# Optimization experiments

Hardware: AMD Instinct MI355X
Metric: run time of the kernel (lower is better)

The kernel has to match this reference:

```python
import jax, jax.numpy as jnp
import numpy as np

N, E, H, L, T = 20000, 160000, 128, 4, 20


def _ln(x, g, b):
    m = jnp.mean(x, -1, keepdims=True)
    v = jnp.mean((x - m) ** 2, -1, keepdims=True)
    return (x - m) * jax.lax.rsqrt(v + 1e-5) * g + b


def _mlp(x, W1, b1, W2, b2, g, b):
    # Linear -> ReLU -> Linear -> LayerNorm, as in mlp_2layer
    h = jax.nn.relu(x @ W1 + b1)
    return _ln(h @ W2 + b2, g, b)


def setup_inputs() -> dict:
    key = jax.random.key(0)
    ks = iter(jax.random.split(key, 64))

    def W(shape):
        fan_in = shape[-2]
        return jax.random.normal(next(ks), shape, jnp.float32) * (fan_in ** -0.5)

    z = lambda s: jnp.zeros(s, jnp.float32)
    o = lambda s: jnp.ones(s, jnp.float32)

    inp = {
        'x': jax.random.normal(next(ks), (N, 12), jnp.float32),
        'edge_attr': jax.random.normal(next(ks), (E, 4), jnp.float32),
        'edge_index': jax.random.randint(next(ks), (2, E), 0, N),
        # node encoder (12 -> H)
        'Wn1': W((12, H)), 'bn1': z((H,)), 'Wn2': W((H, H)), 'bn2': z((H,)), 'gn_ln': o((H,)), 'bn_ln': z((H,)),
        # edge encoder (4 -> H)
        'We1': W((4, H)), 'be1': z((H,)), 'We2': W((H, H)), 'be2': z((H,)), 'ge_ln': o((H,)), 'be_ln': z((H,)),
        # stacked per-layer params: edge_mlp (4H -> H), node_mlp (3H -> H), global_mlp (3H -> H)
        'lEW1': W((L, 4 * H, H)), 'lEb1': z((L, H)), 'lEW2': W((L, H, H)), 'lEb2': z((L, H)), 'lEg': o((L, H)), 'lEbt': z((L, H)),
        'lVW1': W((L, 3 * H, H)), 'lVb1': z((L, H)), 'lVW2': W((L, H, H)), 'lVb2': z((L, H)), 'lVg': o((L, H)), 'lVbt': z((L, H)),
        'lGW1': W((L, 3 * H, H)), 'lGb1': z((L, H)), 'lGW2': W((L, H, H)), 'lGb2': z((L, H)), 'lGg': o((L, H)), 'lGbt': z((L, H)),
        # CNN output head: Conv1d(1->8,k=15,s=4) -> ReLU -> Conv1d(8->1,k=10,s=1)
        'c1w': jax.random.normal(next(ks), (8, 1, 15), jnp.float32) * 0.1, 'c1b': z((8,)),
        'c2w': jax.random.normal(next(ks), (1, 8, 10), jnp.float32) * 0.1, 'c2b': z((1,)),
    }
    return inp


def _forward(x, edge_attr, edge_index,
             Wn1, bn1, Wn2, bn2, gn_ln, bn_ln,
             We1, be1, We2, be2, ge_ln, be_ln,
             lEW1, lEb1, lEW2, lEb2, lEg, lEbt,
             lVW1, lVb1, lVW2, lVb2, lVg, lVbt,
             lGW1, lGb1, lGW2, lGb2, lGg, lGbt,
             c1w, c1b, c2w, c2b):
    senders = edge_index[0]
    receivers = edge_index[1]
    n_nodes = x.shape[0]
    n_edges = edge_attr.shape[0]

    x_v = _mlp(x, Wn1, bn1, Wn2, bn2, gn_ln, bn_ln)          # [N, H]
    x_e = _mlp(edge_attr, We1, be1, We2, be2, ge_ln, be_ln)  # [E, H]
    g = jnp.zeros((1, H), x_v.dtype)                          # B=1 global (no global inputs)

    def step(carry, p):
        x_v, x_e, g = carry
        (EW1, Eb1, EW2, Eb2, Eg, Ebt,
         VW1, Vb1, VW2, Vb2, Vg, Vbt,
         GW1, Gb1, GW2, Gb2, Gg, Gbt) = p
        # edge update: gather sender/receiver feats, concat with edge + global
        g_e = jnp.broadcast_to(g, (n_edges, H))
        edge_in = jnp.concatenate([x_v[senders], x_v[receivers], x_e, g_e], -1)  # [E, 4H]
        x_e = x_e + _mlp(edge_in, EW1, Eb1, EW2, Eb2, Eg, Ebt)
        # node update: sum-aggregate messages by receiver
        aggr = jax.ops.segment_sum(x_e, receivers, num_segments=n_nodes)  # [N, H]
        g_v = jnp.broadcast_to(g, (n_nodes, H))
        node_in = jnp.concatenate([x_v, aggr, g_v], -1)  # [N, 3H]
        x_v = x_v + _mlp(node_in, VW1, Vb1, VW2, Vb2, Vg, Vbt)
        # global update
        g_in = jnp.concatenate([jnp.sum(x_v, 0, keepdims=True), jnp.sum(x_e, 0, keepdims=True), g], -1)  # [1, 3H]
        g = g + _mlp(g_in, GW1, Gb1, GW2, Gb2, Gg, Gbt)
        return (x_v, x_e, g), None

    params = (lEW1, lEb1, lEW2, lEb2, lEg, lEbt,
              lVW1, lVb1, lVW2, lVb2, lVg, lVbt,
              lGW1, lGb1, lGW2, lGb2, lGg, lGbt)
    (x_v, x_e, g), _ = jax.lax.scan(step, (x_v, x_e, g), params)

    # CNN head over the H=128 feature axis -> [N, T]
    dn = ('NCH', 'OIH', 'NCH')
    h = x_v[:, None, :]  # [N, 1, 128]
    h = jax.lax.conv_general_dilated(h, c1w, (4,), 'VALID', dimension_numbers=dn)
    h = jax.nn.relu(h + c1b[None, :, None])  # [N, 8, 29]
    h = jax.lax.conv_general_dilated(h, c2w, (1,), 'VALID', dimension_numbers=dn) + c2b[None, :, None]
    return h[:, 0, :]  # [N, 20]


def reference(x, edge_attr, edge_index,
              Wn1, bn1, Wn2, bn2, gn_ln, bn_ln,
              We1, be1, We2, be2, ge_ln, be_ln,
              lEW1, lEb1, lEW2, lEb2, lEg, lEbt,
              lVW1, lVb1, lVW2, lVb2, lVg, lVbt,
              lGW1, lGb1, lGW2, lGb2, lGg, lGbt,
              c1w, c1b, c2w, c2b):
    return _forward(x, edge_attr, edge_index,
                    Wn1, bn1, Wn2, bn2, gn_ln, bn_ln,
                    We1, be1, We2, be2, ge_ln, be_ln,
                    lEW1, lEb1, lEW2, lEb2, lEg, lEbt,
                    lVW1, lVb1, lVW2, lVb2, lVg, lVbt,
                    lGW1, lGb1, lGW2, lGb2, lGg, lGbt,
                    c1w, c1b, c2w, c2b)
```

## Files before the change

### kernel.cpp

```cpp
#include <hip/hip_runtime.h>

#define NN 20000
#define NE 160000
#define HD 128
#define SA 136

typedef __attribute__((ext_vector_type(8))) short  bfrag;
typedef __attribute__((ext_vector_type(4))) short  s4v;
typedef __attribute__((ext_vector_type(4))) float  facc;
typedef __attribute__((ext_vector_type(4))) float  f4v;

__device__ __forceinline__ float bf2f(unsigned short u){
  union { unsigned int i; float f; } v; v.i = ((unsigned int)u) << 16; return v.f;
}
__device__ __forceinline__ unsigned short f2bf(float f){
  union { float f; unsigned int i; } v; v.f = f;
  unsigned int r = v.i + 0x7fffu + ((v.i >> 16) & 1u);
  return (unsigned short)(r >> 16);
}

__global__ void sentinel_kernel(float* out, float code){
  if (threadIdx.x < 32) out[threadIdx.x] = code;
}

__device__ __forceinline__ void gemm_tile(const short* Ab,
                                          const unsigned short* pk,
                                          int m0, int lane, facc acc[8]){
  const int q = lane >> 4, c = lane & 15;
  #pragma unroll
  for (int kt = 0; kt < 4; ++kt){
    bfrag a = *(const bfrag*)(Ab + (m0 + c) * SA + kt * 32 + q * 8);
    const bfrag* bp = (const bfrag*)pk + kt * 512 + lane;
    #pragma unroll
    for (int nt = 0; nt < 8; ++nt){
      acc[nt] = __builtin_amdgcn_mfma_f32_16x16x32_bf16(a, bp[nt * 64], acc[nt], 0, 0, 0);
    }
  }
}

__device__ __forceinline__ void gemm_tile_h(const short* Ab,
                                            const unsigned short* pk,
                                            int m0, int ntb, int lane, facc acc[4]){
  const int q = lane >> 4, c = lane & 15;
  #pragma unroll
  for (int kt = 0; kt < 4; ++kt){
    bfrag a = *(const bfrag*)(Ab + (m0 + c) * SA + kt * 32 + q * 8);
    const bfrag* bp = (const bfrag*)pk + kt * 512 + ntb * 64 + lane;
    #pragma unroll
    for (int nt = 0; nt < 4; ++nt){
      acc[nt] = __builtin_amdgcn_mfma_f32_16x16x32_bf16(a, bp[nt * 64], acc[nt], 0, 0, 0);
    }
  }
}

__global__ __launch_bounds__(256) void pack_all(
    const float* Wn2, const float* We2,
    const float* lEW1, const float* lEW2,
    const float* lVW1, const float* lVW2,
    unsigned short* packed)
{
  int job = blockIdx.x * 256 + threadIdx.x;
  int mat = job >> 12, r12 = job & 4095;
  int plane = r12 >> 11, r = r12 & 2047;
  int kt = r >> 9, nt = (r >> 6) & 7, lane = r & 63;
  const float* src;
  if (mat == 0) src = Wn2;
  else if (mat == 1) src = We2;
  else {
    int m2 = mat - 2, l = m2 / 7, t = m2 % 7;
    switch (t){
      case 0: src = lEW1 + ((size_t)l*512 +   0)*HD; break;
      case 1: src = lEW1 + ((size_t)l*512 + 128)*HD; break;
      case 2: src = lEW1 + ((size_t)l*512 + 256)*HD; break;
      case 3: src = lEW2 + (size_t)l*HD*HD;          break;
      case 4: src = lVW1 + ((size_t)l*384 +   0)*HD; break;
      case 5: src = lVW1 + ((size_t)l*384 + 128)*HD; break;
      default: src = lVW2 + (size_t)l*HD*HD;         break;
    }
  }
  int krow = kt*32 + (lane>>4)*8, col = nt*16 + (lane&15);
  unsigned short v[8];
  #pragma unroll
  for (int j = 0; j < 8; ++j){
    float w = src[(size_t)(krow + j)*HD + col];
    unsigned short h = f2bf(w);
    v[j] = plane ? f2bf(w - bf2f(h)) : h;
  }
  unsigned short* dst = packed + ((size_t)mat*2 + plane)*16384
                               + ((size_t)(kt*8+nt)*64 + lane)*8;
  #pragma unroll
  for (int j = 0; j < 8; ++j) dst[j] = v[j];
}

__global__ __launch_bounds__(128) void init_small(
    float* g, float* cbe, float* cbv, float* xvs, float* xes,
    const float* Eb1_0, const float* Vb1_0)
{
  int t = threadIdx.x;
  g[t] = 0.f; xvs[t] = 0.f; xes[t] = 0.f;
  cbe[t] = Eb1_0[t]; cbv[t] = Vb1_0[t];
}

__global__ __launch_bounds__(256) void zero_cnt(int* cnt){
  int i = blockIdx.x * 256 + threadIdx.x;
  if (i < NN) cnt[i] = 0;
}
__global__ __launch_bounds__(256) void hist_kernel(const int* eidx, int* cnt){
  int e = blockIdx.x * 256 + threadIdx.x;
  atomicAdd(&cnt[eidx[NE + e]], 1);
}
__global__ __launch_bounds__(1024) void scan_kernel(const int* cnt, int* base, int* ofs){
  __shared__ int wsum[16];
  int t = threadIdx.x, lane = t & 63;
  int vals[20]; int loc = 0;
  if (t < 1000){
    #pragma unroll
    for (int k = 0; k < 20; ++k){ vals[k] = cnt[t*20 + k]; loc += vals[k]; }
  }
  int inc = loc;
  #pragma unroll
  for (int d = 1; d < 64; d <<= 1){ int o = __shfl_up(inc, d); if (lane >= d) inc += o; }
  if (lane == 63) wsum[t >> 6] = inc;
  __syncthreads();
  if (t < 16){
    int v = wsum[t];
    #pragma unroll
    for (int d = 1; d < 16; d <<= 1){ int o = __shfl_up(v, d); if (t >= d) v += o; }
    wsum[t] = v;
  }
  __syncthreads();
  int woff = (t >= 64) ? wsum[(t >> 6) - 1] : 0;
  int run = woff + inc - loc;
  if (t < 1000){
    #pragma unroll
    for (int k = 0; k < 20; ++k){ base[t*20 + k] = run; ofs[t*20 + k] = run; run += vals[k]; }
  }
  if (t == 0) base[NN] = NE;
}
__global__ __launch_bounds__(256) void scatter_kernel(const int* eidx, int* ofs,
                                                      int* perm, int* ssid, int* srid){
  int e = blockIdx.x * 256 + threadIdx.x;
  int s = eidx[e], r = eidx[NE + e];
  int pos = atomicAdd(&ofs[r], 1);
  perm[pos] = e; ssid[pos] = s; srid[pos] = r;
}

__global__ __launch_bounds__(256) void enc_node(
    const float* x, const float* W1, const float* b1,
    const unsigned short* pkW2, const float* b2,
    const float* gl, const float* bl, float* xvf, int nrows)
{
  __shared__ float inb[64*12];
  __shared__ __align__(16) short Hh[64*SA];
  __shared__ __align__(16) short Hl[64*SA];
  int tid = threadIdx.x, r0 = blockIdx.x * 64;
  for (int j = tid; j < 64*12; j += 256){
    int rr = j / 12, k = j % 12, rg = r0 + rr;
    inb[j] = (rg < nrows) ? x[(size_t)rg*12 + k] : 0.f;
  }
  __syncthreads();
  {
    int cc = tid & 127;
    float w1c[12];
    #pragma unroll
    for (int k = 0; k < 12; ++k) w1c[k] = W1[k*HD + cc];
    float bb = b1[cc];
    for (int it = 0; it < 32; ++it){
      int rr = it*2 + (tid >> 7);
      float a = bb;
      #pragma unroll
      for (int k = 0; k < 12; ++k) a += inb[rr*12 + k] * w1c[k];
      float h = fmaxf(a, 0.f);
      unsigned short hh = f2bf(h);
      Hh[rr*SA + cc] = (short)hh;
      Hl[rr*SA + cc] = (short)f2bf(h - bf2f(hh));
    }
  }
  __syncthreads();
  int lane = tid & 63, q = lane >> 4, c = lane & 15, m0 = (tid >> 6) * 16;
  facc a2[8];
  #pragma unroll
  for (int nt = 0; nt < 8; ++nt) a2[nt] = (facc){0.f,0.f,0.f,0.f};
  gemm_tile(Hh, pkW2,         m0, lane, a2);
  gemm_tile(Hl, pkW2,         m0, lane, a2);
  gemm_tile(Hh, pkW2 + 16384, m0, lane, a2);
  #pragma unroll
  for (int i = 0; i < 4; ++i){
    int rl = m0 + q*4 + i, rg = r0 + rl;
    float vals[8], s = 0.f, ss = 0.f;
    #pragma unroll
    for (int nt = 0; nt < 8; ++nt){
      float v = a2[nt][i] + b2[nt*16 + c];
      vals[nt] = v; s += v; ss += v*v;
    }
    s += __shfl_xor(s,1); ss += __shfl_xor(ss,1);
    s += __shfl_xor(s,2); ss += __shfl_xor(ss,2);
    s += __shfl_xor(s,4); ss += __shfl_xor(ss,4);
    s += __shfl_xor(s,8); ss += __shfl_xor(ss,8);
    float mean = s * 0.0078125f;
    float var  = ss * 0.0078125f - mean*mean;
    float rs   = rsqrtf(var + 1e-5f);
    if (rg < nrows){
      #pragma unroll
      for (int nt = 0; nt < 8; ++nt){
        int col = nt*16 + c;
        xvf[(size_t)rg*HD + col] = (vals[nt]-mean)*rs*gl[col] + bl[col];
      }
    }
  }
}

__global__ __launch_bounds__(256) void enc_edge(
    const float* ea, const int* perm, const float* W1, const float* b1,
    const unsigned short* pkW2, const float* b2,
    const float* gl, const float* bl, unsigned short* xeb)
{
  __shared__ float inb[64*4];
  __shared__ __align__(16) short Hh[64*SA];
  __shared__ __align__(16) short Hl[64*SA];
  int tid = threadIdx.x, r0 = blockIdx.x * 64;
  {
    int rr = tid >> 2, k = tid & 3;
    int pe = perm[r0 + rr];
    inb[tid] = ea[(size_t)pe*4 + k];
  }
  __syncthreads();
  {
    int cc = tid & 127;
    float w0 = W1[0*HD+cc], w1 = W1[1*HD+cc], w2 = W1[2*HD+cc], w3 = W1[3*HD+cc];
    float bb = b1[cc];
    for (int it = 0; it < 32; ++it){
      int rr = it*2 + (tid >> 7);
      float a = bb + inb[rr*4+0]*w0 + inb[rr*4+1]*w1 + inb[rr*4+2]*w2 + inb[rr*4+3]*w3;
      float h = fmaxf(a, 0.f);
      unsigned short hh = f2bf(h);
      Hh[rr*SA + cc] = (short)hh;
      Hl[rr*SA + cc] = (short)f2bf(h - bf2f(hh));
    }
  }
  __syncthreads();
  int lane = tid & 63, q = lane >> 4, c = lane & 15, m0 = (tid >> 6) * 16;
  facc a2[8];
  #pragma unroll
  for (int nt = 0; nt < 8; ++nt) a2[nt] = (facc){0.f,0.f,0.f,0.f};
  gemm_tile(Hh, pkW2,         m0, lane, a2);
  gemm_tile(Hl, pkW2,         m0, lane, a2);
  gemm_tile(Hh, pkW2 + 16384, m0, lane, a2);
  #pragma unroll
  for (int i = 0; i < 4; ++i){
    int rl = m0 + q*4 + i, rg = r0 + rl;
    float vals[8], s = 0.f, ss = 0.f;
    #pragma unroll
    for (int nt = 0; nt < 8; ++nt){
      float v = a2[nt][i] + b2[nt*16 + c];
      vals[nt] = v; s += v; ss += v*v;
    }
    s += __shfl_xor(s,1); ss += __shfl_xor(ss,1);
    s += __shfl_xor(s,2); ss += __shfl_xor(ss,2);
    s += __shfl_xor(s,4); ss += __shfl_xor(ss,4);
    s += __shfl_xor(s,8); ss += __shfl_xor(ss,8);
    float mean = s * 0.0078125f;
    float var  = ss * 0.0078125f - mean*mean;
    float rs   = rsqrtf(var + 1e-5f);
    #pragma unroll
    for (int nt = 0; nt < 8; ++nt){
      int col = nt*16 + c;
      xeb[(size_t)rg*HD + col] = f2bf((vals[nt]-mean)*rs*gl[col] + bl[col]);
    }
  }
}

__global__ __launch_bounds__(512, 4) void pq_kernel(
    const float* xvf, const unsigned short* pkA, const unsigned short* pkB,
    unsigned short* P, unsigned short* Q, int nrows)
{
  __shared__ __align__(16) short Ah[64*SA];
  __shared__ __align__(16) short Al[64*SA];
  int tid = threadIdx.x, r0 = blockIdx.x * 64;
  for (int j = tid; j < 1024; j += 512){
    int rr = j >> 4, ch = j & 15, rg = r0 + rr;
    float v[8];
    if (rg < nrows){
      f4v a = *(const f4v*)(xvf + (size_t)rg*HD + ch*8);
      f4v b = *(const f4v*)(xvf + (size_t)rg*HD + ch*8 + 4);
      v[0]=a[0];v[1]=a[1];v[2]=a[2];v[3]=a[3];v[4]=b[0];v[5]=b[1];v[6]=b[2];v[7]=b[3];
    } else {
      #pragma unroll
      for (int k = 0; k < 8; ++k) v[k] = 0.f;
    }
    short* dh = Ah + rr*SA + ch*8;
    short* dl = Al + rr*SA + ch*8;
    #pragma unroll
    for (int k = 0; k < 8; ++k){
      unsigned short h = f2bf(v[k]);
      dh[k] = (short)h; dl[k] = (short)f2bf(v[k] - bf2f(h));
    }
  }
  __syncthreads();
  int lane = tid & 63, wq = tid >> 6, q = lane >> 4, c = lane & 15;
  int m0 = (wq & 3) * 16, ntb = (wq >> 2) * 4;
  facc ap[4], aq[4];
  #pragma unroll
  for (int nt = 0; nt < 4; ++nt){ ap[nt] = (facc){0.f,0.f,0.f,0.f}; aq[nt] = (facc){0.f,0.f,0.f,0.f}; }
  gemm_tile_h(Ah, pkA,         m0, ntb, lane, ap);
  gemm_tile_h(Al, pkA,         m0, ntb, lane, ap);
  gemm_tile_h(Ah, pkA + 16384, m0, ntb, lane, ap);
  gemm_tile_h(Ah, pkB,         m0, ntb, lane, aq);
  gemm_tile_h(Al, pkB,         m0, ntb, lane, aq);
  gemm_tile_h(Ah, pkB + 16384, m0, ntb, lane, aq);
  #pragma unroll
  for (int i = 0; i < 4; ++i){
    int rl = m0 + q*4 + i, rg = r0 + rl;
    if (rg < nrows){
      s4v pv, qv;
      #pragma unroll
      for (int nt = 0; nt < 4; ++nt){
        pv[nt] = (short)f2bf(ap[nt][i]);
        qv[nt] = (short)f2bf(aq[nt][i]);
      }
      *(s4v*)(P + (size_t)rg*HD + c*8 + ntb) = pv;
      *(s4v*)(Q + (size_t)rg*HD + c*8 + ntb) = qv;
    }
  }
}

__global__ __launch_bounds__(512, 4) void edge_kernel(
    unsigned short* xeb, const int* ssid, const int* srid,
    const unsigned short* P, const unsigned short* Q, const float* cbe,
    const unsigned short* pkW1c, const unsigned short* pkW2,
    const float* Eb2, const float* Eg, const float* Ebt)
{
  __shared__ __align__(16) short Ab[64*SA];
  __shared__ __align__(16) short Hl[64*SA];
  __shared__ float lnS[128], lnSS[128];
  int tid = threadIdx.x, e0 = blockIdx.x * 64;
  int lane = tid & 63, wq = tid >> 6, q = lane >> 4, c = lane & 15;
  int m0 = (wq & 3) * 16, ntb = (wq >> 2) * 4, half = wq >> 2;

  int sid[4], rid[4];
  #pragma unroll
  for (int i = 0; i < 4; ++i){
    int rl = m0 + q*4 + i;
    sid[i] = ssid[e0 + rl];
    rid[i] = srid[e0 + rl];
  }
  s4v psv[4], qrv[4];
  #pragma unroll
  for (int i = 0; i < 4; ++i){
    psv[i] = *(const s4v*)(P + (size_t)sid[i]*HD + c*8 + ntb);
    qrv[i] = *(const s4v*)(Q + (size_t)rid[i]*HD + c*8 + ntb);
  }

  for (int j = tid; j < 1024; j += 512){
    int rr = j >> 4, ch = j & 15;
    *(bfrag*)(Ab + rr*SA + ch*8) = *(const bfrag*)(xeb + (size_t)(e0+rr)*HD + ch*8);
  }
  __syncthreads();

  unsigned int rres[4][2];
  #pragma unroll
  for (int i = 0; i < 4; ++i){
    int rl = m0 + q*4 + i;
    #pragma unroll
    for (int p2 = 0; p2 < 2; ++p2){
      unsigned short a0 = (unsigned short)Ab[rl*SA + (ntb + 2*p2    )*16 + c];
      unsigned short a1 = (unsigned short)Ab[rl*SA + (ntb + 2*p2 + 1)*16 + c];
      rres[i][p2] = ((unsigned int)a1 << 16) | a0;
    }
  }
  float cb[4];
  #pragma unroll
  for (int nt = 0; nt < 4; ++nt) cb[nt] = cbe[(ntb + nt)*16 + c];
  float pg[4][4];
  #pragma unroll
  for (int i = 0; i < 4; ++i){
    #pragma unroll
    for (int nt = 0; nt < 4; ++nt)
      pg[i][nt] = bf2f((unsigned short)psv[i][nt]) + bf2f((unsigned short)qrv[i][nt]) + cb[nt];
  }
  facc acc[4];
  #pragma unroll
  for (int nt = 0; nt < 4; ++nt) acc[nt] = (facc){0.f,0.f,0.f,0.f};
  gemm_tile_h(Ab, pkW1c,         m0, ntb, lane, acc);
  gemm_tile_h(Ab, pkW1c + 16384, m0, ntb, lane, acc);
  __syncthreads();
  #pragma unroll
  for (int i = 0; i < 4; ++i){
    int rl = m0 + q*4 + i;
    #pragma unroll
    for (int nt = 0; nt < 4; ++nt){
      int col = (ntb + nt)*16 + c;
      float h = fmaxf(acc[nt][i] + pg[i][nt], 0.f);
      unsigned short hh = f2bf(h);
      Ab[rl*SA + col] = (short)hh;
      Hl[rl*SA + col] = (short)f2bf(h - bf2f(hh));
    }
  }
  __syncthreads();
  facc a2[4];
  #pragma unroll
  for (int nt = 0; nt < 4; ++nt) a2[nt] = (facc){0.f,0.f,0.f,0.f};
  gemm_tile_h(Ab, pkW2,         m0, ntb, lane, a2);
  gemm_tile_h(Hl, pkW2,         m0, ntb, lane, a2);
  gemm_tile_h(Ab, pkW2 + 16384, m0, ntb, lane, a2);
  float vals[4][4], myS[4], mySS[4];
  #pragma unroll
  for (int i = 0; i < 4; ++i){
    int rl = m0 + q*4 + i;
    float s = 0.f, ss = 0.f;
    #pragma unroll
    for (int nt = 0; nt < 4; ++nt){
      float v = a2[nt][i] + Eb2[(ntb + nt)*16 + c];
      vals[i][nt] = v; s += v; ss += v*v;
    }
    s += __shfl_xor(s,1); ss += __shfl_xor(ss,1);
    s += __shfl_xor(s,2); ss += __shfl_xor(ss,2);
    s += __shfl_xor(s,4); ss += __shfl_xor(ss,4);
    s += __shfl_xor(s,8); ss += __shfl_xor(ss,8);
    myS[i] = s; mySS[i] = ss;
    if (c == 0){ lnS[rl*2 + half] = s; lnSS[rl*2 + half] = ss; }
  }
  __syncthreads();
  #pragma unroll
  for (int i = 0; i < 4; ++i){
    int rl = m0 + q*4 + i, eg = e0 + rl;
    float sT  = myS[i]  + lnS[rl*2 + (half^1)];
    float ssT = mySS[i] + lnSS[rl*2 + (half^1)];
    float mean = sT * 0.0078125f;
    float var  = ssT * 0.0078125f - mean*mean;
    float rs   = rsqrtf(var + 1e-5f);
    #pragma unroll
    for (int nt = 0; nt < 4; ++nt){
      int col = (ntb + nt)*16 + c;
      float o = (vals[i][nt]-mean)*rs*Eg[col] + Ebt[col];
      float rv = bf2f((unsigned short)(rres[i][nt >> 1] >> ((nt & 1)*16)));
      xeb[(size_t)eg*HD + col] = f2bf(rv + o);
    }
  }
}

__global__ __launch_bounds__(256, 4) void node_kernel(
    float* xvf, const unsigned short* xeb, const int* base, const float* cbv,
    const unsigned short* pkW1a, const unsigned short* pkW1b, const unsigned short* pkW2,
    const float* Vb2, const float* Vg, const float* Vbt,
    float* xv_sum, float* xes, int do_xes,
    const unsigned short* pkAn, const unsigned short* pkBn,
    unsigned short* P, unsigned short* Q, int do_pq, int nrows)
{
  __shared__ __align__(16) short Avh[32*SA];
  __shared__ __align__(16) short Avl[32*SA];
  __shared__ __align__(16) short Agh[32*SA];
  __shared__ __align__(16) short Agl[32*SA];
  __shared__ float red[128];
  __shared__ float lnS[64], lnSS[64];
  int tid = threadIdx.x, r0 = blockIdx.x * 32;
  int lane = tid & 63, wq = tid >> 6;
  if (tid < 128) red[tid] = 0.f;
  __syncthreads();
  for (int j = tid; j < 512; j += 256){
    int rr = j >> 4, ch = j & 15, rg = r0 + rr;
    float v[8];
    if (rg < nrows){
      f4v a = *(const f4v*)(xvf + (size_t)rg*HD + ch*8);
      f4v b = *(const f4v*)(xvf + (size_t)rg*HD + ch*8 + 4);
      v[0]=a[0];v[1]=a[1];v[2]=a[2];v[3]=a[3];v[4]=b[0];v[5]=b[1];v[6]=b[2];v[7]=b[3];
    } else {
      #pragma unroll
      for (int k = 0; k < 8; ++k) v[k] = 0.f;
    }
    short *dvh = Avh + rr*SA + ch*8, *dvl = Avl + rr*SA + ch*8;
    #pragma unroll
    for (int k = 0; k < 8; ++k){
      unsigned short h1 = f2bf(v[k]);
      dvh[k] = (short)h1; dvl[k] = (short)f2bf(v[k] - bf2f(h1));
    }
  }
  float xp0 = 0.f, xp1 = 0.f;
  for (int j = 0; j < 8; ++j){
    int rl = wq*8 + j, rg = r0 + rl;
    float s0 = 0.f, s1 = 0.f;
    if (rg < nrows){
      int b0 = base[rg], b1 = base[rg + 1];
      int e = b0;
      for (; e + 1 < b1; e += 2){
        unsigned int u0 = *(const unsigned int*)(xeb + (size_t)e*HD + lane*2);
        unsigned int u1 = *(const unsigned int*)(xeb + (size_t)(e+1)*HD + lane*2);
        s0 += bf2f((unsigned short)(u0 & 0xffffu)) + bf2f((unsigned short)(u1 & 0xffffu));
        s1 += bf2f((unsigned short)(u0 >> 16))     + bf2f((unsigned short)(u1 >> 16));
      }
      if (e < b1){
        unsigned int u0 = *(const unsigned int*)(xeb + (size_t)e*HD + lane*2);
        s0 += bf2f((unsigned short)(u0 & 0xffffu));
        s1 += bf2f((unsigned short)(u0 >> 16));
      }
    }
    unsigned short h0 = f2bf(s0), h1 = f2bf(s1);
    unsigned short l0 = f2bf(s0 - bf2f(h0)), l1 = f2bf(s1 - bf2f(h1));
    *(unsigned int*)(Agh + rl*SA + 2*lane) = ((unsigned int)h1 << 16) | h0;
    *(unsigned int*)(Agl + rl*SA + 2*lane) = ((unsigned int)l1 << 16) | l0;
    xp0 += s0; xp1 += s1;
  }
  if (do_xes){
    atomicAdd(&red[lane*2],     xp0);
    atomicAdd(&red[lane*2 + 1], xp1);
  }
  __syncthreads();
  if (do_xes && tid < 128) atomicAdd(&xes[tid], red[tid]);
  int q = lane >> 4, c = lane & 15;
  int m0 = (wq & 1) * 16, ntb = (wq >> 1) * 4, half = wq >> 1;
  facc acc[4];
  #pragma unroll
  for (int nt = 0; nt < 4; ++nt) acc[nt] = (facc){0.f,0.f,0.f,0.f};
  gemm_tile_h(Avh, pkW1a,         m0, ntb, lane, acc);
  gemm_tile_h(Avl, pkW1a,         m0, ntb, lane, acc);
  gemm_tile_h(Avh, pkW1a + 16384, m0, ntb, lane, acc);
  gemm_tile_h(Agh, pkW1b,         m0, ntb, lane, acc);
  gemm_tile_h(Agl, pkW1b,         m0, ntb, lane, acc);
  gemm_tile_h(Agh, pkW1b + 16384, m0, ntb, lane, acc);
  __syncthreads();
  #pragma unroll
  for (int i = 0; i < 4; ++i){
    int rl = m0 + q*4 + i;
    #pragma unroll
    for (int nt = 0; nt < 4; ++nt){
      int col = (ntb + nt)*16 + c;
      float h = fmaxf(acc[nt][i] + cbv[col], 0.f);
      unsigned short hh = f2bf(h);
      Avh[rl*SA + col] = (short)hh;
      Avl[rl*SA + col] = (short)f2bf(h - bf2f(hh));
    }
  }
  __syncthreads();
  facc a2[4];
  #pragma unroll
  for (int nt = 0; nt < 4; ++nt) a2[nt] = (facc){0.f,0.f,0.f,0.f};
  gemm_tile_h(Avh, pkW2,         m0, ntb, lane, a2);
  gemm_tile_h(Avl, pkW2,         m0, ntb, lane, a2);
  gemm_tile_h(Avh, pkW2 + 16384, m0, ntb, lane, a2);
  float vals[4][4], myS[4], mySS[4];
  #pragma unroll
  for (int i = 0; i < 4; ++i){
    int rl = m0 + q*4 + i;
    float s = 0.f, ss = 0.f;
    #pragma unroll
    for (int nt = 0; nt < 4; ++nt){
      float v = a2[nt][i] + Vb2[(ntb + nt)*16 + c];
      vals[i][nt] = v; s += v; ss += v*v;
    }
    s += __shfl_xor(s,1); ss += __shfl_xor(ss,1);
    s += __shfl_xor(s,2); ss += __shfl_xor(ss,2);
    s += __shfl_xor(s,4); ss += __shfl_xor(ss,4);
    s += __shfl_xor(s,8); ss += __shfl_xor(ss,8);
    myS[i] = s; mySS[i] = ss;
    if (c == 0){ lnS[rl*2 + half] = s; lnSS[rl*2 + half] = ss; }
  }
  __syncthreads();
  float csum[4] = {0.f,0.f,0.f,0.f};
  #pragma unroll
  for (int i = 0; i < 4; ++i){
    int rl = m0 + q*4 + i, rg = r0 + rl;
    float sT  = myS[i]  + lnS[rl*2 + (half^1)];
    float ssT = mySS[i] + lnSS[rl*2 + (half^1)];
    float mean = sT * 0.0078125f;
    float var  = ssT * 0.0078125f - mean*mean;
    float rs   = rsqrtf(var + 1e-5f);
    if (rg < nrows){
      #pragma unroll
      for (int nt = 0; nt < 4; ++nt){
        int col = (ntb + nt)*16 + c;
        float o = (vals[i][nt]-mean)*rs*Vg[col] + Vbt[col];
        size_t gi = (size_t)rg*HD + col;
        float nv = xvf[gi] + o;
        xvf[gi] = nv;
        csum[nt] += nv;
        if (do_pq){
          unsigned short hh = f2bf(nv);
          Agh[rl*SA + col] = (short)hh;
          Agl[rl*SA + col] = (short)f2bf(nv - bf2f(hh));
        }
      }
    }
  }
  #pragma unroll
  for (int nt = 0; nt < 4; ++nt){
    float v = csum[nt]; v += __shfl_xor(v,16); v += __shfl_xor(v,32);
    if (q == 0) atomicAdd(&xv_sum[(ntb + nt)*16 + c], v);
  }
  if (do_pq){
    __syncthreads();
    facc ap[4], aq[4];
    #pragma unroll
    for (int nt = 0; nt < 4; ++nt){ ap[nt] = (facc){0.f,0.f,0.f,0.f}; aq[nt] = (facc){0.f,0.f,0.f,0.f}; }
    gemm_tile_h(Agh, pkAn,         m0, ntb, lane, ap);
    gemm_tile_h(Agl, pkAn,         m0, ntb, lane, ap);
    gemm_tile_h(Agh, pkAn + 16384, m0, ntb, lane, ap);
    gemm_tile_h(Agh, pkBn,         m0, ntb, lane, aq);
    gemm_tile_h(Agl, pkBn,         m0, ntb, lane, aq);
    gemm_tile_h(Agh, pkBn + 16384, m0, ntb, lane, aq);
    #pragma unroll
    for (int i = 0; i < 4; ++i){
      int rl = m0 + q*4 + i, rg = r0 + rl;
      if (rg < nrows){
        s4v pv, qv;
        #pragma unroll
        for (int nt = 0; nt < 4; ++nt){
          pv[nt] = (short)f2bf(ap[nt][i]);
          qv[nt] = (short)f2bf(aq[nt][i]);
        }
        *(s4v*)(P + (size_t)rg*HD + c*8 + ntb) = pv;
        *(s4v*)(Q + (size_t)rg*HD + c*8 + ntb) = qv;
      }
    }
  }
}

__global__ __launch_bounds__(1024) void g_kernel(
    float* xvs, float* xes, float* g,
    const float* GW1, const float* Gb1, const float* GW2, const float* Gb2,
    const float* Gg, const float* Gbt,
    float* cbe, float* cbv,
    const float* EW1n, const float* Eb1n, const float* VW1n, const float* Vb1n)
{
  __shared__ float gin[384], h1[128], gn[128], red[4];
  __shared__ float partA[8][128], partB[8][128];
  int tid = threadIdx.x, t = tid & 127, kk = tid >> 7;
  if (tid < 384) gin[tid] = (tid < 128) ? xvs[tid] : (tid < 256) ? xes[tid-128] : g[tid-256];
  __syncthreads();
  {
    float a = 0.f;
    for (int k = kk*48; k < kk*48 + 48; ++k) a += gin[k] * GW1[(size_t)k*HD + t];
    partA[kk][t] = a;
  }
  __syncthreads();
  if (kk == 0){
    float a = Gb1[t];
    #pragma unroll
    for (int i = 0; i < 8; ++i) a += partA[i][t];
    h1[t] = fmaxf(a, 0.f);
  }
  __syncthreads();
  {
    float o = 0.f;
    for (int k = kk*16; k < kk*16 + 16; ++k) o += h1[k] * GW2[(size_t)k*HD + t];
    partA[kk][t] = o;
  }
  __syncthreads();
  float oo = 0.f;
  if (kk == 0){
    oo = Gb2[t];
    #pragma unroll
    for (int i = 0; i < 8; ++i) oo += partA[i][t];
  }
  __syncthreads();
  if (tid < 128){
    float s = oo;
    #pragma unroll
    for (int d = 1; d < 64; d <<= 1) s += __shfl_xor(s, d);
    if ((tid & 63) == 0) red[tid >> 6] = s;
  }
  __syncthreads();
  float mean = (red[0] + red[1]) * 0.0078125f;
  if (tid < 128){
    float dd = oo - mean;
    float v = dd * dd;
    #pragma unroll
    for (int d = 1; d < 64; d <<= 1) v += __shfl_xor(v, d);
    if ((tid & 63) == 0) red[2 + (tid >> 6)] = v;
  }
  __syncthreads();
  if (tid < 128){
    float rs = rsqrtf((red[2] + red[3]) * 0.0078125f + 1e-5f);
    float gnv = g[tid] + (oo - mean)*rs*Gg[tid] + Gbt[tid];
    g[tid] = gnv; gn[tid] = gnv;
    xvs[tid] = 0.f; xes[tid] = 0.f;
  }
  __syncthreads();
  {
    float ce = 0.f, cv = 0.f;
    for (int k = kk*16; k < kk*16 + 16; ++k){
      ce += gn[k] * EW1n[(size_t)k*HD + t];
      cv += gn[k] * VW1n[(size_t)k*HD + t];
    }
    partA[kk][t] = ce; partB[kk][t] = cv;
  }
  __syncthreads();
  if (kk == 0){
    float ce = Eb1n[t], cv = Vb1n[t];
    #pragma unroll
    for (int i = 0; i < 8; ++i){ ce += partA[i][t]; cv += partB[i][t]; }
    cbe[t] = ce; cbv[t] = cv;
  }
}

__global__ __launch_bounds__(256) void decoder_kernel(
    const float* xv, const float* c1w, const float* c1b,
    const float* c2w, const float* c2b, float* out)
{
  __shared__ float xl[4][128];
  __shared__ float hl[4][232];
  __shared__ float w1[120], b1[8], w2[80];
  __shared__ float b2s;
  int tid = threadIdx.x, nl = tid >> 6, t = tid & 63;
  int n = blockIdx.x * 4 + nl;
  if (tid < 120) w1[tid] = c1w[tid];
  else if (tid < 128) b1[tid - 120] = c1b[tid - 120];
  else if (tid < 208) w2[tid - 128] = c2w[tid - 128];
  else if (tid == 208) b2s = c2b[0];
  xl[nl][t]      = xv[(size_t)n*HD + t];
  xl[nl][t + 64] = xv[(size_t)n*HD + 64 + t];
  __syncthreads();
  for (int j = t; j < 232; j += 64){
    int ch = j / 29, pp = j % 29;
    float a = b1[ch];
    #pragma unroll
    for (int u = 0; u < 15; ++u) a += xl[nl][4*pp + u] * w1[ch*15 + u];
    hl[nl][j] = fmaxf(a, 0.f);
  }
  __syncthreads();
  if (t < 20){
    float o = b2s;
    #pragma unroll
    for (int ch = 0; ch < 8; ++ch)
      #pragma unroll
      for (int u = 0; u < 10; ++u)
        o += hl[nl][ch*29 + t + u] * w2[ch*10 + u];
    out[(size_t)n*20 + t] = o;
  }
}

extern "C" void kernel_launch(void* const* d_in, const int* in_sizes, int n_in,
                              void* d_out, int out_size, void* d_ws, size_t ws_size,
                              hipStream_t stream)
{
  const float* x    = (const float*)d_in[0];
  const float* ea   = (const float*)d_in[1];
  const int*   eidx = (const int*)d_in[2];
  const float* Wn1  = (const float*)d_in[3];  const float* bn1  = (const float*)d_in[4];
  const float* Wn2  = (const float*)d_in[5];  const float* bn2  = (const float*)d_in[6];
  const float* gnln = (const float*)d_in[7];  const float* bnln = (const float*)d_in[8];
  const float* We1  = (const float*)d_in[9];  const float* be1  = (const float*)d_in[10];
  const float* We2  = (const float*)d_in[11]; const float* be2  = (const float*)d_in[12];
  const float* geln = (const float*)d_in[13]; const float* beln = (const float*)d_in[14];
  const float* lEW1 = (const float*)d_in[15]; const float* lEb1 = (const float*)d_in[16];
  const float* lEW2 = (const float*)d_in[17]; const float* lEb2 = (const float*)d_in[18];
  const float* lEg  = (const float*)d_in[19]; const float* lEbt = (const float*)d_in[20];
  const float* lVW1 = (const float*)d_in[21]; const float* lVb1 = (const float*)d_in[22];
  const float* lVW2 = (const float*)d_in[23]; const float* lVb2 = (const float*)d_in[24];
  const float* lVg  = (const float*)d_in[25]; const float* lVbt = (const float*)d_in[26];
  const float* lGW1 = (const float*)d_in[27]; const float* lGb1 = (const float*)d_in[28];
  const float* lGW2 = (const float*)d_in[29]; const float* lGb2 = (const float*)d_in[30];
  const float* lGg  = (const float*)d_in[31]; const float* lGbt = (const float*)d_in[32];
  const float* c1w  = (const float*)d_in[33]; const float* c1b  = (const float*)d_in[34];
  const float* c2w  = (const float*)d_in[35]; const float* c2b  = (const float*)d_in[36];

  char* ws = (char*)d_ws;
  size_t off = 0;
  auto alloc = [&](size_t b){ size_t o = off; off += (b + 255) & ~(size_t)255; return o; };
  unsigned short* pk   = (unsigned short*)(ws + alloc((size_t)30*2*16384*2));
  float*          g    = (float*)(ws + alloc(512));
  float*          cbe  = (float*)(ws + alloc(512));
  float*          cbv  = (float*)(ws + alloc(512));
  float*          xvs  = (float*)(ws + alloc(512));
  float*          xes  = (float*)(ws + alloc(512));
  float*          xvf  = (float*)(ws + alloc((size_t)NN*HD*4));
  unsigned short* P    = (unsigned short*)(ws + alloc((size_t)NN*HD*2));
  unsigned short* Q    = (unsigned short*)(ws + alloc((size_t)NN*HD*2));
  unsigned short* xeb  = (unsigned short*)(ws + alloc((size_t)NE*HD*2));
  int*            cnt  = (int*)(ws + alloc((size_t)NN*4));
  int*            bse  = (int*)(ws + alloc((size_t)(NN+1)*4));
  int*            ofs  = (int*)(ws + alloc((size_t)NN*4));
  int*            perm = (int*)(ws + alloc((size_t)NE*4));
  int*            ssid = (int*)(ws + alloc((size_t)NE*4));
  int*            srid = (int*)(ws + alloc((size_t)NE*4));

  if (ws_size < off){
    sentinel_kernel<<<1, 32, 0, stream>>>((float*)d_out, 20000.f + (float)(ws_size >> 20));
    return;
  }

  auto slot = [&](int m){ return pk + (size_t)m * 32768; };

  pack_all<<<480, 256, 0, stream>>>(Wn2, We2, lEW1, lEW2, lVW1, lVW2, pk);
  init_small<<<1, 128, 0, stream>>>(g, cbe, cbv, xvs, xes, lEb1, lVb1);
  zero_cnt<<<(NN + 255)/256, 256, 0, stream>>>(cnt);
  hist_kernel<<<NE/256, 256, 0, stream>>>(eidx, cnt);
  scan_kernel<<<1, 1024, 0, stream>>>(cnt, bse, ofs);
  scatter_kernel<<<NE/256, 256, 0, stream>>>(eidx, ofs, perm, ssid, srid);

  enc_node<<<(NN + 63)/64, 256, 0, stream>>>(x, Wn1, bn1, slot(0), bn2, gnln, bnln, xvf, NN);
  enc_edge<<<NE/64, 256, 0, stream>>>(ea, perm, We1, be1, slot(1), be2, geln, beln, xeb);

  pq_kernel<<<(NN + 63)/64, 512, 0, stream>>>(xvf, slot(2), slot(3), P, Q, NN);

  for (int l = 0; l < 4; ++l){
    int m = 2 + 7*l;
    edge_kernel<<<NE/64, 512, 0, stream>>>(xeb, ssid, srid, P, Q, cbe,
        slot(m+2), slot(m+3),
        lEb2 + (size_t)l*HD, lEg + (size_t)l*HD, lEbt + (size_t)l*HD);
    node_kernel<<<(NN + 31)/32, 256, 0, stream>>>(xvf, xeb, bse, cbv,
        slot(m+4), slot(m+5), slot(m+6),
        lVb2 + (size_t)l*HD, lVg + (size_t)l*HD, lVbt + (size_t)l*HD,
        xvs, xes, (l < 3) ? 1 : 0,
        slot(m+7), slot(m+8), P, Q, (l < 3) ? 1 : 0, NN);
    if (l < 3){
      g_kernel<<<1, 1024, 0, stream>>>(xvs, xes, g,
          lGW1 + (size_t)l*384*HD, lGb1 + (size_t)l*HD,
          lGW2 + (size_t)l*HD*HD, lGb2 + (size_t)l*HD,
          lGg + (size_t)l*HD, lGbt + (size_t)l*HD,
          cbe, cbv,
          lEW1 + ((size_t)(l+1)*512 + 384)*HD, lEb1 + (size_t)(l+1)*HD,
          lVW1 + ((size_t)(l+1)*384 + 256)*HD, lVb1 + (size_t)(l+1)*HD);
    }
  }
  decoder_kernel<<<NN/4, 256, 0, stream>>>(xvf, c1w, c1b, c2w, c2b, (float*)d_out);

  hipError_t e = hipGetLastError();
  if (e != hipSuccess){
    sentinel_kernel<<<1, 32, 0, stream>>>((float*)d_out, 10000.f + (float)e);
  }
  (void)in_sizes; (void)n_in; (void)out_size;
}
```

Measured before the change: 819.0 us.

## Halve edge kernel waves, each wave computes two row tiles sharing B fragments

The edge MLP kernel now runs 4 waves per 64-edge block instead of 8. Each wave covers 32 rows with two accumulator sets, so every loaded weight fragment feeds two MFMAs. This halves global/L2 weight-fragment traffic per block and cuts per-wave overhead, at the cost of higher register pressure (launch bounds relaxed to 256,3) and less latency hiding from fewer waves.

```diff
diff --git a/kernel.cpp b/kernel.cpp
--- a/kernel.cpp
+++ b/kernel.cpp
@@ -49,6 +49,25 @@
     #pragma unroll
     for (int nt = 0; nt < 4; ++nt){
       acc[nt] = __builtin_amdgcn_mfma_f32_16x16x32_bf16(a, bp[nt * 64], acc[nt], 0, 0, 0);
+    }
+  }
+}
+
+__device__ __forceinline__ void gemm_tile_h2(const short* Ab,
+                                             const unsigned short* pk,
+                                             int m0, int ntb, int lane,
+                                             facc acc0[4], facc acc1[4]){
+  const int q = lane >> 4, c = lane & 15;
+  #pragma unroll
+  for (int kt = 0; kt < 4; ++kt){
+    bfrag a0 = *(const bfrag*)(Ab + (m0 +      c) * SA + kt * 32 + q * 8);
+    bfrag a1 = *(const bfrag*)(Ab + (m0 + 16 + c) * SA + kt * 32 + q * 8);
+    const bfrag* bp = (const bfrag*)pk + kt * 512 + ntb * 64 + lane;
+    #pragma unroll
+    for (int nt = 0; nt < 4; ++nt){
+      bfrag b = bp[nt * 64];
+      acc0[nt] = __builtin_amdgcn_mfma_f32_16x16x32_bf16(a0, b, acc0[nt], 0, 0, 0);
+      acc1[nt] = __builtin_amdgcn_mfma_f32_16x16x32_bf16(a1, b, acc1[nt], 0, 0, 0);
     }
   }
 }
@@ -324,7 +343,7 @@
   }
 }
 
-__global__ __launch_bounds__(512, 4) void edge_kernel(
+__global__ __launch_bounds__(256, 3) void edge_kernel(
     unsigned short* xeb, const int* ssid, const int* srid,
     const unsigned short* P, const unsigned short* Q, const float* cbe,
     const unsigned short* pkW1c, const unsigned short* pkW2,
@@ -335,106 +354,115 @@
   __shared__ float lnS[128], lnSS[128];
   int tid = threadIdx.x, e0 = blockIdx.x * 64;
   int lane = tid & 63, wq = tid >> 6, q = lane >> 4, c = lane & 15;
-  int m0 = (wq & 3) * 16, ntb = (wq >> 2) * 4, half = wq >> 2;
-
-  int sid[4], rid[4];
-  #pragma unroll
-  for (int i = 0; i < 4; ++i){
-    int rl = m0 + q*4 + i;
-    sid[i] = ssid[e0 + rl];
-    rid[i] = srid[e0 + rl];
-  }
-  s4v psv[4], qrv[4];
-  #pragma unroll
-  for (int i = 0; i < 4; ++i){
-    psv[i] = *(const s4v*)(P + (size_t)sid[i]*HD + c*8 + ntb);
-    qrv[i] = *(const s4v*)(Q + (size_t)rid[i]*HD + c*8 + ntb);
-  }
-
-  for (int j = tid; j < 1024; j += 512){
+  int m0 = (wq & 1) * 32, ntb = (wq >> 1) * 4, half = wq >> 1;
+
+  float pg[2][4][4];
+  {
+    float cb[4];
+    #pragma unroll
+    for (int nt = 0; nt < 4; ++nt) cb[nt] = cbe[(ntb + nt)*16 + c];
+    #pragma unroll
+    for (int rs = 0; rs < 2; ++rs){
+      #pragma unroll
+      for (int i = 0; i < 4; ++i){
+        int rl = m0 + rs*16 + q*4 + i;
+        int sid = ssid[e0 + rl], rid = srid[e0 + rl];
+        s4v ps = *(const s4v*)(P + (size_t)sid*HD + c*8 + ntb);
+        s4v qr = *(const s4v*)(Q + (size_t)rid*HD + c*8 + ntb);
+        #pragma unroll
+        for (int nt = 0; nt < 4; ++nt)
+          pg[rs][i][nt] = bf2f((unsigned short)ps[nt]) + bf2f((unsigned short)qr[nt]) + cb[nt];
+      }
+    }
+  }
+
+  for (int j = tid; j < 1024; j += 256){
     int rr = j >> 4, ch = j & 15;
     *(bfrag*)(Ab + rr*SA + ch*8) = *(const bfrag*)(xeb + (size_t)(e0+rr)*HD + ch*8);
   }
   __syncthreads();
 
-  unsigned int rres[4][2];
-  #pragma unroll
-  for (int i = 0; i < 4; ++i){
-    int rl = m0 + q*4 + i;
-    #pragma unroll
-    for (int p2 = 0; p2 < 2; ++p2){
-      unsigned short a0 = (unsigned short)Ab[rl*SA + (ntb + 2*p2    )*16 + c];
-      unsigned short a1 = (unsigned short)Ab[rl*SA + (ntb + 2*p2 + 1)*16 + c];
-      rres[i][p2] = ((unsigned int)a1 << 16) | a0;
-    }
-  }
-  float cb[4];
-  #pragma unroll
-  for (int nt = 0; nt < 4; ++nt) cb[nt] = cbe[(ntb + nt)*16 + c];
-  float pg[4][4];
-  #pragma unroll
-  for (int i = 0; i < 4; ++i){
-    #pragma unroll
-    for (int nt = 0; nt < 4; ++nt)
-      pg[i][nt] = bf2f((unsigned short)psv[i][nt]) + bf2f((unsigned short)qrv[i][nt]) + cb[nt];
-  }
-  facc acc[4];
-  #pragma unroll
-  for (int nt = 0; nt < 4; ++nt) acc[nt] = (facc){0.f,0.f,0.f,0.f};
-  gemm_tile_h(Ab, pkW1c,         m0, ntb, lane, acc);
-  gemm_tile_h(Ab, pkW1c + 16384, m0, ntb, lane, acc);
-  __syncthreads();
-  #pragma unroll
-  for (int i = 0; i < 4; ++i){
-    int rl = m0 + q*4 + i;
-    #pragma unroll
-    for (int nt = 0; nt < 4; ++nt){
-      int col = (ntb + nt)*16 + c;
-      float h = fmaxf(acc[nt][i] + pg[i][nt], 0.f);
-      unsigned short hh = f2bf(h);
-      Ab[rl*SA + col] = (short)hh;
-      Hl[rl*SA + col] = (short)f2bf(h - bf2f(hh));
-    }
-  }
-  __syncthreads();
-  facc a2[4];
-  #pragma unroll
-  for (int nt = 0; nt < 4; ++nt) a2[nt] = (facc){0.f,0.f,0.f,0.f};
-  gemm_tile_h(Ab, pkW2,         m0, ntb, lane, a2);
-  gemm_tile_h(Hl, pkW2,         m0, ntb, lane, a2);
-  gemm_tile_h(Ab, pkW2 + 16384, m0, ntb, lane, a2);
-  float vals[4][4], myS[4], mySS[4];
-  #pragma unroll
-  for (int i = 0; i < 4; ++i){
-    int rl = m0 + q*4 + i;
-    float s = 0.f, ss = 0.f;
-    #pragma unroll
-    for (int nt = 0; nt < 4; ++nt){
-      float v = a2[nt][i] + Eb2[(ntb + nt)*16 + c];
-      vals[i][nt] = v; s += v; ss += v*v;
-    }
-    s += __shfl_xor(s,1); ss += __shfl_xor(ss,1);
-    s += __shfl_xor(s,2); ss += __shfl_xor(ss,2);
-    s += __shfl_xor(s,4); ss += __shfl_xor(ss,4);
-    s += __shfl_xor(s,8); ss += __shfl_xor(ss,8);
-    myS[i] = s; mySS[i] = ss;
-    if (c == 0){ lnS[rl*2 + half] = s; lnSS[rl*2 + half] = ss; }
-  }
-  __syncthreads();
-  #pragma unroll
-  for (int i = 0; i < 4; ++i){
-    int rl = m0 + q*4 + i, eg = e0 + rl;
-    float sT  = myS[i]  + lnS[rl*2 + (half^1)];
-    float ssT = mySS[i] + lnSS[rl*2 + (half^1)];
-    float mean = sT * 0.0078125f;
-    float var  = ssT * 0.0078125f - mean*mean;
-    float rs   = rsqrtf(var + 1e-5f);
-    #pragma unroll
-    for (int nt = 0; nt < 4; ++nt){
-      int col = (ntb + nt)*16 + c;
-      float o = (vals[i][nt]-mean)*rs*Eg[col] + Ebt[col];
-      float rv = bf2f((unsigned short)(rres[i][nt >> 1] >> ((nt & 1)*16)));
-      xeb[(size_t)eg*HD + col] = f2bf(rv + o);
+  unsigned int rres[2][4][2];
+  #pragma unroll
+  for (int rs = 0; rs < 2; ++rs){
+    #pragma unroll
+    for (int i = 0; i < 4; ++i){
+      int rl = m0 + rs*16 + q*4 + i;
+      #pragma unroll
+      for (int p2 = 0; p2 < 2; ++p2){
+        unsigned short a0 = (unsigned short)Ab[rl*SA + (ntb + 2*p2    )*16 + c];
+        unsigned short a1 = (unsigned short)Ab[rl*SA + (ntb + 2*p2 + 1)*16 + c];
+        rres[rs][i][p2] = ((unsigned int)a1 << 16) | a0;
+      }
+    }
+  }
+  facc acc0[4], acc1[4];
+  #pragma unroll
+  for (int nt = 0; nt < 4; ++nt){ acc0[nt] = (facc){0.f,0.f,0.f,0.f}; acc1[nt] = (facc){0.f,0.f,0.f,0.f}; }
+  gemm_tile_h2(Ab, pkW1c,         m0, ntb, lane, acc0, acc1);
+  gemm_tile_h2(Ab, pkW1c + 16384, m0, ntb, lane, acc0, acc1);
+  __syncthreads();
+  #pragma unroll
+  for (int rs = 0; rs < 2; ++rs){
+    #pragma unroll
+    for (int i = 0; i < 4; ++i){
+      int rl = m0 + rs*16 + q*4 + i;
+      #pragma unroll
+      for (int nt = 0; nt < 4; ++nt){
+        int col = (ntb + nt)*16 + c;
+        float av = rs ? acc1[nt][i] : acc0[nt][i];
+        float h = fmaxf(av + pg[rs][i][nt], 0.f);
+        unsigned short hh = f2bf(h);
+        Ab[rl*SA + col] = (short)hh;
+        Hl[rl*SA + col] = (short)f2bf(h - bf2f(hh));
+      }
+    }
+  }
+  __syncthreads();
+  facc a20[4], a21[4];
+  #pragma unroll
+  for (int nt = 0; nt < 4; ++nt){ a20[nt] = (facc){0.f,0.f,0.f,0.f}; a21[nt] = (facc){0.f,0.f,0.f,0.f}; }
+  gemm_tile_h2(Ab, pkW2,         m0, ntb, lane, a20, a21);
+  gemm_tile_h2(Hl, pkW2,         m0, ntb, lane, a20, a21);
+  gemm_tile_h2(Ab, pkW2 + 16384, m0, ntb, lane, a20, a21);
+  float vals[2][4][4], myS[2][4], mySS[2][4];
+  #pragma unroll
+  for (int rs = 0; rs < 2; ++rs){
+    #pragma unroll
+    for (int i = 0; i < 4; ++i){
+      int rl = m0 + rs*16 + q*4 + i;
+      float s = 0.f, ss = 0.f;
+      #pragma unroll
+      for (int nt = 0; nt < 4; ++nt){
+        float v = (rs ? a21[nt][i] : a20[nt][i]) + Eb2[(ntb + nt)*16 + c];
+        vals[rs][i][nt] = v; s += v; ss += v*v;
+      }
+      s += __shfl_xor(s,1); ss += __shfl_xor(ss,1);
+      s += __shfl_xor(s,2); ss += __shfl_xor(ss,2);
+      s += __shfl_xor(s,4); ss += __shfl_xor(ss,4);
+      s += __shfl_xor(s,8); ss += __shfl_xor(ss,8);
+      myS[rs][i] = s; mySS[rs][i] = ss;
+      if (c == 0){ lnS[rl*2 + half] = s; lnSS[rl*2 + half] = ss; }
+    }
+  }
+  __syncthreads();
+  #pragma unroll
+  for (int rs = 0; rs < 2; ++rs){
+    #pragma unroll
+    for (int i = 0; i < 4; ++i){
+      int rl = m0 + rs*16 + q*4 + i, eg = e0 + rl;
+      float sT  = myS[rs][i]  + lnS[rl*2 + (half^1)];
+      float ssT = mySS[rs][i] + lnSS[rl*2 + (half^1)];
+      float mean = sT * 0.0078125f;
+      float var  = ssT * 0.0078125f - mean*mean;
+      float rs2  = rsqrtf(var + 1e-5f);
+      #pragma unroll
+      for (int nt = 0; nt < 4; ++nt){
+        int col = (ntb + nt)*16 + c;
+        float o = (vals[rs][i][nt]-mean)*rs2*Eg[col] + Ebt[col];
+        float rv = bf2f((unsigned short)(rres[rs][i][nt >> 1] >> ((nt & 1)*16)));
+        xeb[(size_t)eg*HD + col] = f2bf(rv + o);
+      }
     }
   }
 }
@@ -794,7 +822,7 @@
 
   for (int l = 0; l < 4; ++l){
     int m = 2 + 7*l;
-    edge_kernel<<<NE/64, 512, 0, stream>>>(xeb, ssid, srid, P, Q, cbe,
+    edge_kernel<<<NE/64, 256, 0, stream>>>(xeb, ssid, srid, P, Q, cbe,
         slot(m+2), slot(m+3),
         lEb2 + (size_t)l*HD, lEg + (size_t)l*HD, lEbt + (size_t)l*HD);
     node_kernel<<<(NN + 31)/32, 256, 0, stream>>>(xvf, xeb, bse, cbv,
```

After: 799.3 us. 2.4% less time.
